# Performance work log

Measured on AMD Instinct MI355X. Metric: run time of the kernel, lower is better.

Reference implementation:

```python
import jax, jax.numpy as jnp
import numpy as np

N = 100000
E = 1600000
F = 64
OUT = 7

def setup_inputs() -> dict:
    key = jax.random.key(0)
    k1, k2, k3, k4, k5 = jax.random.split(key, 5)
    x = jax.random.normal(k1, (N, F), dtype=jnp.float32)
    edge_index = jax.random.randint(k2, (2, E), 0, N, dtype=jnp.int64)
    W_l = jax.random.normal(k3, (F, OUT), dtype=jnp.float32) / np.sqrt(F)
    b_l = jax.random.normal(k4, (OUT,), dtype=jnp.float32) * 0.01
    W_r = jax.random.normal(k5, (F, OUT), dtype=jnp.float32) / np.sqrt(F)
    return {"x": x, "edge_index": edge_index, "W_l": W_l, "b_l": b_l, "W_r": W_r}

def reference(x, edge_index, W_l, b_l, W_r):
    # PyG SAGEConv (mean aggr): out = lin_l(mean_{j in N(i)} x_j) + lin_r(x_i), then relu
    src, dst = edge_index[0], edge_index[1]
    msgs = x[src]                                            # [E, F] gather
    agg = jax.ops.segment_sum(msgs, dst, num_segments=N)     # [N, F]
    cnt = jax.ops.segment_sum(jnp.ones((E,), dtype=x.dtype), dst, num_segments=N)
    mean = agg / jnp.maximum(cnt, 1.0)[:, None]              # isolated nodes -> 0
    out = mean @ W_l + b_l + x @ W_r                         # [N, 7]
    return jax.nn.relu(out)
```

## Files before the change

### kernel.cpp

```cpp
#include <hip/hip_runtime.h>

#define NN 100000
#define NE 1600000
#define FIN 64
#define FOUT 7

#define BSH 9
#define BMASK 511u
#define NB  196
#define CAP 9216
#define PBLK 512
#define PTH  512
#define EPB (NE / PBLK)
#define EPT ((EPB + PTH - 1) / PTH)
#define SPLIT 2
#define ATH 512
#define HCAP 4608
#define APT 10

__device__ __forceinline__ unsigned bf16r(float f) {
    unsigned u = __float_as_uint(f);
    return (u + 0x7fffu + ((u >> 16) & 1u)) >> 16;
}
__device__ __forceinline__ float bflo(unsigned u) { return __uint_as_float(u << 16); }
__device__ __forceinline__ float bfhi(unsigned u) { return __uint_as_float(u & 0xffff0000u); }

__global__ __launch_bounds__(256) void proj_kernel(
    const float* __restrict__ x, const float* __restrict__ Wl,
    const float* __restrict__ bl, const float* __restrict__ Wr,
    unsigned* __restrict__ z, float* __restrict__ outself, int n)
{
    __shared__ float sW[2 * FIN * FOUT + FOUT];
    for (int t = threadIdx.x; t < FIN * FOUT; t += blockDim.x) {
        sW[t] = Wl[t];
        sW[FIN * FOUT + t] = Wr[t];
    }
    if (threadIdx.x < FOUT) sW[2 * FIN * FOUT + threadIdx.x] = bl[threadIdx.x];
    __syncthreads();

    int i = blockIdx.x * blockDim.x + threadIdx.x;
    if (i >= n) return;

    float al[FOUT], ar[FOUT];
#pragma unroll
    for (int j = 0; j < FOUT; ++j) { al[j] = 0.f; ar[j] = 0.f; }

    const float4* xr = (const float4*)(x + (size_t)i * FIN);
#pragma unroll
    for (int kk = 0; kk < FIN / 4; ++kk) {
        float4 xv = xr[kk];
        float v[4] = {xv.x, xv.y, xv.z, xv.w};
#pragma unroll
        for (int c = 0; c < 4; ++c) {
            int k = kk * 4 + c;
#pragma unroll
            for (int j = 0; j < FOUT; ++j) {
                al[j] = fmaf(v[c], sW[k * FOUT + j], al[j]);
                ar[j] = fmaf(v[c], sW[FIN * FOUT + k * FOUT + j], ar[j]);
            }
        }
    }

    uint4 pk;
    pk.x = bf16r(al[0]) | (bf16r(al[1]) << 16);
    pk.y = bf16r(al[2]) | (bf16r(al[3]) << 16);
    pk.z = bf16r(al[4]) | (bf16r(al[5]) << 16);
    pk.w = bf16r(al[6]);
    ((uint4*)z)[i] = pk;

    float* o = outself + (size_t)i * FOUT;
#pragma unroll
    for (int j = 0; j < FOUT; ++j)
        o[j] = ar[j] + sW[2 * FIN * FOUT + j];
}

__global__ __launch_bounds__(PTH) void part_kernel(
    const int* __restrict__ eg, int* __restrict__ gcur,
    unsigned* __restrict__ part)
{
    __shared__ unsigned st_rank[NB];
    __shared__ unsigned st_scan[256];
    __shared__ unsigned st_start[NB];
    __shared__ unsigned st_gbase[NB];
    __shared__ unsigned stage[EPB];
    __shared__ unsigned char bof[EPB];

    const int t  = threadIdx.x;
    const int e0 = blockIdx.x * EPB;

    for (int b = t; b < NB; b += PTH) st_rank[b] = 0;
    __syncthreads();

    unsigned held[EPT], hbr[EPT];
    int nh = 0;
#pragma unroll
    for (int j = 0; j < EPT; ++j) {
        int k = t + j * PTH;
        if (k < EPB) {
            unsigned s = (unsigned)eg[e0 + k];
            unsigned d = (unsigned)eg[NE + e0 + k];
            unsigned b = d >> BSH;
            unsigned r = atomicAdd(&st_rank[b], 1u);
            held[nh] = ((d & BMASK) << 17) | s;
            hbr[nh]  = (b << 16) | r;
            ++nh;
        }
    }
    __syncthreads();

    if (t < 256) st_scan[t] = (t < NB) ? st_rank[t] : 0u;
    __syncthreads();
    for (int off = 1; off < 256; off <<= 1) {
        unsigned v = 0;
        if (t < 256 && t >= off) v = st_scan[t - off];
        __syncthreads();
        if (t < 256) st_scan[t] += v;
        __syncthreads();
    }
    if (t < NB) {
        unsigned cnt = st_rank[t];
        st_start[t] = st_scan[t] - cnt;
        st_gbase[t] = cnt ? (unsigned)atomicAdd(&gcur[t], (int)cnt) : 0u;
    }
    __syncthreads();

    for (int j = 0; j < nh; ++j) {
        unsigned b = hbr[j] >> 16, r = hbr[j] & 0xffffu;
        unsigned pos = st_start[b] + r;
        stage[pos] = held[j];
        bof[pos]   = (unsigned char)b;
    }
    __syncthreads();

    for (int j = t; j < EPB; j += PTH) {
        unsigned b = bof[j];
        unsigned idx = st_gbase[b] + (unsigned)j - st_start[b];
        if (idx < CAP) part[(size_t)b * CAP + idx] = stage[j];
    }
}

__global__ __launch_bounds__(ATH) void acc_kernel(
    const int* __restrict__ gcur, const unsigned* __restrict__ part,
    const unsigned* __restrict__ zb, float* __restrict__ partial)
{
    __shared__ unsigned s_cnt[512];
    __shared__ unsigned s_scan[512];
    __shared__ unsigned sstage[HCAP];

    const int t = threadIdx.x;
    const int b = blockIdx.x >> 1;
    const int s = blockIdx.x & 1;

    s_cnt[t] = 0;
    __syncthreads();

    int cnt = gcur[b];
    if (cnt > CAP) cnt = CAP;
    int beg = s ? (cnt >> 1) : 0;
    int end = s ? cnt : (cnt >> 1);
    const unsigned* ep = part + (size_t)b * CAP;

    unsigned hsrc[APT], hnr[APT];
    int nh = 0;
#pragma unroll
    for (int j = 0; j < APT; ++j) {
        int k = beg + t + j * ATH;
        if (k < end) {
            unsigned e = ep[k];
            unsigned node = e >> 17;
            unsigned r = atomicAdd(&s_cnt[node], 1u);
            hsrc[nh] = e & 0x1FFFFu;
            hnr[nh]  = (node << 16) | r;
            ++nh;
        }
    }
    __syncthreads();

    s_scan[t] = s_cnt[t];
    __syncthreads();
    for (int off = 1; off < 512; off <<= 1) {
        unsigned v = (t >= off) ? s_scan[t - off] : 0u;
        __syncthreads();
        s_scan[t] += v;
        __syncthreads();
    }

    for (int j = 0; j < nh; ++j) {
        unsigned node = hnr[j] >> 16, r = hnr[j] & 0xffffu;
        sstage[(s_scan[node] - s_cnt[node]) + r] = hsrc[j];
    }
    unsigned mydeg  = s_cnt[t];
    unsigned mybase = s_scan[t] - mydeg;
    __syncthreads();

    float a0 = 0.f, a1 = 0.f, a2 = 0.f, a3 = 0.f, a4 = 0.f, a5 = 0.f, a6 = 0.f;
    for (unsigned j = 0; j < mydeg; ++j) {
        unsigned src = sstage[mybase + j];
        uint4 zr = ((const uint4*)zb)[src];
        a0 += bflo(zr.x); a1 += bfhi(zr.x);
        a2 += bflo(zr.y); a3 += bfhi(zr.y);
        a4 += bflo(zr.z); a5 += bfhi(zr.z);
        a6 += bflo(zr.w);
    }

    float* pp = partial + ((size_t)blockIdx.x * 512 + t) * 8;
    *(float4*)(pp)     = make_float4(a0, a1, a2, a3);
    *(float4*)(pp + 4) = make_float4(a4, a5, a6, (float)mydeg);
}

__global__ __launch_bounds__(256) void merge_kernel(
    const float* __restrict__ partial, float* __restrict__ out, int n)
{
    int i = blockIdx.x * blockDim.x + threadIdx.x;
    if (i >= n) return;
    int b = i >> BSH;
    int t = i & (int)BMASK;
    const float4* p0 = (const float4*)(partial + ((size_t)(b * 2    ) * 4096) + t * 8);
    const float4* p1 = (const float4*)(partial + ((size_t)(b * 2 + 1) * 4096) + t * 8);
    float4 a = p0[0], c = p0[1];
    float4 d = p1[0], e = p1[1];
    float s0 = a.x + d.x, s1 = a.y + d.y, s2 = a.z + d.z, s3 = a.w + d.w;
    float s4 = c.x + e.x, s5 = c.y + e.y, s6 = c.z + e.z;
    float r = 1.0f / fmaxf(c.w + e.w, 1.0f);
    float* o = out + (size_t)i * FOUT;
    o[0] = fmaxf(fmaf(s0, r, o[0]), 0.f);
    o[1] = fmaxf(fmaf(s1, r, o[1]), 0.f);
    o[2] = fmaxf(fmaf(s2, r, o[2]), 0.f);
    o[3] = fmaxf(fmaf(s3, r, o[3]), 0.f);
    o[4] = fmaxf(fmaf(s4, r, o[4]), 0.f);
    o[5] = fmaxf(fmaf(s5, r, o[5]), 0.f);
    o[6] = fmaxf(fmaf(s6, r, o[6]), 0.f);
}

extern "C" void kernel_launch(void* const* d_in, const int* in_sizes, int n_in,
                              void* d_out, int out_size, void* d_ws, size_t ws_size,
                              hipStream_t stream) {
    const float* x   = (const float*)d_in[0];
    const int*   edg = (const int*)d_in[1];
    const float* Wl  = (const float*)d_in[2];
    const float* bl  = (const float*)d_in[3];
    const float* Wr  = (const float*)d_in[4];
    float* out = (float*)d_out;

    unsigned* z       = (unsigned*)d_ws;
    unsigned* part    = z + (size_t)NN * 4;
    float*    partial = (float*)(part + (size_t)NB * CAP);
    int*      gcur    = (int*)(partial + (size_t)NB * SPLIT * 4096);

    hipMemsetAsync(gcur, 0, NB * sizeof(int), stream);

    proj_kernel<<<(NN + 255) / 256, 256, 0, stream>>>(x, Wl, bl, Wr, z, out, NN);
    part_kernel<<<PBLK, PTH, 0, stream>>>(edg, gcur, part);
    acc_kernel<<<NB * SPLIT, ATH, 0, stream>>>(gcur, part, z, partial);
    merge_kernel<<<(NN + 255) / 256, 256, 0, stream>>>(partial, out, NN);
}
```

Measured before the change: 128.2 us.

## Fuse merge into accumulation kernel using one 1024-thread block per bucket

The accumulation kernel now handles a whole destination bucket in one 1024-thread block. Each node's edge list is split between two threads, and the halves are combined through shared memory. The mean, residual add and ReLU are applied in place, so the separate merge kernel and the global partial buffer go away, saving a launch and the partial-sum round trip. The projection kernel also drops its shared-memory weight staging and reads the weights directly through cached global loads. In exchange, each acc block uses much more LDS and only 196 blocks are launched, which lowers parallelism on a large GPU.

```diff
diff --git a/kernel.cpp b/kernel.cpp
--- a/kernel.cpp
+++ b/kernel.cpp
@@ -13,10 +13,8 @@
 #define PTH  512
 #define EPB (NE / PBLK)
 #define EPT ((EPB + PTH - 1) / PTH)
-#define SPLIT 2
-#define ATH 512
-#define HCAP 4608
-#define APT 10
+#define ATH 1024
+#define APT ((CAP + ATH - 1) / ATH)
 
 __device__ __forceinline__ unsigned bf16r(float f) {
     unsigned u = __float_as_uint(f);
@@ -30,14 +28,6 @@
     const float* __restrict__ bl, const float* __restrict__ Wr,
     unsigned* __restrict__ z, float* __restrict__ outself, int n)
 {
-    __shared__ float sW[2 * FIN * FOUT + FOUT];
-    for (int t = threadIdx.x; t < FIN * FOUT; t += blockDim.x) {
-        sW[t] = Wl[t];
-        sW[FIN * FOUT + t] = Wr[t];
-    }
-    if (threadIdx.x < FOUT) sW[2 * FIN * FOUT + threadIdx.x] = bl[threadIdx.x];
-    __syncthreads();
-
     int i = blockIdx.x * blockDim.x + threadIdx.x;
     if (i >= n) return;
 
@@ -55,8 +45,8 @@
             int k = kk * 4 + c;
 #pragma unroll
             for (int j = 0; j < FOUT; ++j) {
-                al[j] = fmaf(v[c], sW[k * FOUT + j], al[j]);
-                ar[j] = fmaf(v[c], sW[FIN * FOUT + k * FOUT + j], ar[j]);
+                al[j] = fmaf(v[c], Wl[k * FOUT + j], al[j]);
+                ar[j] = fmaf(v[c], Wr[k * FOUT + j], ar[j]);
             }
         }
     }
@@ -71,7 +61,7 @@
     float* o = outself + (size_t)i * FOUT;
 #pragma unroll
     for (int j = 0; j < FOUT; ++j)
-        o[j] = ar[j] + sW[2 * FIN * FOUT + j];
+        o[j] = ar[j] + bl[j];
 }
 
 __global__ __launch_bounds__(PTH) void part_kernel(
@@ -141,31 +131,29 @@
 
 __global__ __launch_bounds__(ATH) void acc_kernel(
     const int* __restrict__ gcur, const unsigned* __restrict__ part,
-    const unsigned* __restrict__ zb, float* __restrict__ partial)
+    const unsigned* __restrict__ zb, float* __restrict__ out)
 {
     __shared__ unsigned s_cnt[512];
     __shared__ unsigned s_scan[512];
-    __shared__ unsigned sstage[HCAP];
+    __shared__ unsigned sstage[CAP];
+    __shared__ float    lacc[512 * 8];
 
     const int t = threadIdx.x;
-    const int b = blockIdx.x >> 1;
-    const int s = blockIdx.x & 1;
-
-    s_cnt[t] = 0;
+    const int b = blockIdx.x;
+
+    if (t < 512) s_cnt[t] = 0;
     __syncthreads();
 
     int cnt = gcur[b];
     if (cnt > CAP) cnt = CAP;
-    int beg = s ? (cnt >> 1) : 0;
-    int end = s ? cnt : (cnt >> 1);
     const unsigned* ep = part + (size_t)b * CAP;
 
     unsigned hsrc[APT], hnr[APT];
     int nh = 0;
 #pragma unroll
     for (int j = 0; j < APT; ++j) {
-        int k = beg + t + j * ATH;
-        if (k < end) {
+        int k = t + j * ATH;
+        if (k < cnt) {
             unsigned e = ep[k];
             unsigned node = e >> 17;
             unsigned r = atomicAdd(&s_cnt[node], 1u);
@@ -176,26 +164,33 @@
     }
     __syncthreads();
 
-    s_scan[t] = s_cnt[t];
+    if (t < 512) s_scan[t] = s_cnt[t];
     __syncthreads();
     for (int off = 1; off < 512; off <<= 1) {
-        unsigned v = (t >= off) ? s_scan[t - off] : 0u;
-        __syncthreads();
-        s_scan[t] += v;
-        __syncthreads();
-    }
+        unsigned v = 0;
+        if (t < 512 && t >= off) v = s_scan[t - off];
+        __syncthreads();
+        if (t < 512) s_scan[t] += v;
+        __syncthreads();
+    }
+    __syncthreads();
 
     for (int j = 0; j < nh; ++j) {
         unsigned node = hnr[j] >> 16, r = hnr[j] & 0xffffu;
         sstage[(s_scan[node] - s_cnt[node]) + r] = hsrc[j];
     }
-    unsigned mydeg  = s_cnt[t];
-    unsigned mybase = s_scan[t] - mydeg;
-    __syncthreads();
+    __syncthreads();
+
+    unsigned node = t & 511u;
+    unsigned half = t >> 9;
+    unsigned deg  = s_cnt[node];
+    unsigned base = s_scan[node] - deg;
+    unsigned lo = half ? (deg >> 1) : 0u;
+    unsigned hi = half ? deg : (deg >> 1);
 
     float a0 = 0.f, a1 = 0.f, a2 = 0.f, a3 = 0.f, a4 = 0.f, a5 = 0.f, a6 = 0.f;
-    for (unsigned j = 0; j < mydeg; ++j) {
-        unsigned src = sstage[mybase + j];
+    for (unsigned j = lo; j < hi; ++j) {
+        unsigned src = sstage[base + j];
         uint4 zr = ((const uint4*)zb)[src];
         a0 += bflo(zr.x); a1 += bfhi(zr.x);
         a2 += bflo(zr.y); a3 += bfhi(zr.y);
@@ -203,33 +198,30 @@
         a6 += bflo(zr.w);
     }
 
-    float* pp = partial + ((size_t)blockIdx.x * 512 + t) * 8;
-    *(float4*)(pp)     = make_float4(a0, a1, a2, a3);
-    *(float4*)(pp + 4) = make_float4(a4, a5, a6, (float)mydeg);
-}
-
-__global__ __launch_bounds__(256) void merge_kernel(
-    const float* __restrict__ partial, float* __restrict__ out, int n)
-{
-    int i = blockIdx.x * blockDim.x + threadIdx.x;
-    if (i >= n) return;
-    int b = i >> BSH;
-    int t = i & (int)BMASK;
-    const float4* p0 = (const float4*)(partial + ((size_t)(b * 2    ) * 4096) + t * 8);
-    const float4* p1 = (const float4*)(partial + ((size_t)(b * 2 + 1) * 4096) + t * 8);
-    float4 a = p0[0], c = p0[1];
-    float4 d = p1[0], e = p1[1];
-    float s0 = a.x + d.x, s1 = a.y + d.y, s2 = a.z + d.z, s3 = a.w + d.w;
-    float s4 = c.x + e.x, s5 = c.y + e.y, s6 = c.z + e.z;
-    float r = 1.0f / fmaxf(c.w + e.w, 1.0f);
-    float* o = out + (size_t)i * FOUT;
-    o[0] = fmaxf(fmaf(s0, r, o[0]), 0.f);
-    o[1] = fmaxf(fmaf(s1, r, o[1]), 0.f);
-    o[2] = fmaxf(fmaf(s2, r, o[2]), 0.f);
-    o[3] = fmaxf(fmaf(s3, r, o[3]), 0.f);
-    o[4] = fmaxf(fmaf(s4, r, o[4]), 0.f);
-    o[5] = fmaxf(fmaf(s5, r, o[5]), 0.f);
-    o[6] = fmaxf(fmaf(s6, r, o[6]), 0.f);
+    if (half) {
+        float* L = &lacc[node * 8];
+        *(float4*)(L)     = make_float4(a0, a1, a2, a3);
+        *(float4*)(L + 4) = make_float4(a4, a5, a6, 0.f);
+    }
+    __syncthreads();
+
+    if (!half) {
+        const float* L = &lacc[node * 8];
+        a0 += L[0]; a1 += L[1]; a2 += L[2]; a3 += L[3];
+        a4 += L[4]; a5 += L[5]; a6 += L[6];
+        int i = (b << BSH) + (int)node;
+        if (i < NN) {
+            float r = 1.0f / (float)max((int)deg, 1);
+            float* o = out + (size_t)i * FOUT;
+            o[0] = fmaxf(fmaf(a0, r, o[0]), 0.f);
+            o[1] = fmaxf(fmaf(a1, r, o[1]), 0.f);
+            o[2] = fmaxf(fmaf(a2, r, o[2]), 0.f);
+            o[3] = fmaxf(fmaf(a3, r, o[3]), 0.f);
+            o[4] = fmaxf(fmaf(a4, r, o[4]), 0.f);
+            o[5] = fmaxf(fmaf(a5, r, o[5]), 0.f);
+            o[6] = fmaxf(fmaf(a6, r, o[6]), 0.f);
+        }
+    }
 }
 
 extern "C" void kernel_launch(void* const* d_in, const int* in_sizes, int n_in,
@@ -242,15 +234,13 @@
     const float* Wr  = (const float*)d_in[4];
     float* out = (float*)d_out;
 
-    unsigned* z       = (unsigned*)d_ws;
-    unsigned* part    = z + (size_t)NN * 4;
-    float*    partial = (float*)(part + (size_t)NB * CAP);
-    int*      gcur    = (int*)(partial + (size_t)NB * SPLIT * 4096);
+    unsigned* z    = (unsigned*)d_ws;
+    unsigned* part = z + (size_t)NN * 4;
+    int*      gcur = (int*)(part + (size_t)NB * CAP);
 
     hipMemsetAsync(gcur, 0, NB * sizeof(int), stream);
 
     proj_kernel<<<(NN + 255) / 256, 256, 0, stream>>>(x, Wl, bl, Wr, z, out, NN);
     part_kernel<<<PBLK, PTH, 0, stream>>>(edg, gcur, part);
-    acc_kernel<<<NB * SPLIT, ATH, 0, stream>>>(gcur, part, z, partial);
-    merge_kernel<<<(NN + 255) / 256, 256, 0, stream>>>(partial, out, NN);
-}
+    acc_kernel<<<NB, ATH, 0, stream>>>(gcur, part, z, out);
+}
```

Result: no change. 127.9 us (-0.2%).
